# Kernel optimization log

Hardware: AMD Instinct MI355X
Metric: run time of the kernel (lower is better)

Reference implementation:

```python
import jax, jax.numpy as jnp
import numpy as np

B = 64       # number of graphs
R = 148      # fixed ROI count from source
D = 64       # hidden_channels (embed_dim, 4 heads)
H = 4
IN1 = 64     # node feature dim (after stripping label column)
INR = 148    # roi-graph feature dim
HID = 1000
NCLS = 2
N1 = 262144
E1 = 1048576
N2 = B * R
E2 = 262144
EPS = 1e-5


def setup_inputs() -> dict:
    key = jax.random.key(0)
    ks = jax.random.split(key, 40)
    def p(i, shape, s=0.1):
        return jax.random.normal(ks[i], shape, dtype=jnp.float32) * s
    inp = {
        'x_feat': jax.random.normal(ks[0], (N1, IN1), dtype=jnp.float32),
        'node_roi': jax.random.randint(ks[1], (N1,), 0, R, dtype=jnp.int32),
        'batch1': ((jnp.arange(N1, dtype=jnp.int32) * B) // N1).astype(jnp.int32),
        'edge_index1': jax.random.randint(ks[2], (2, E1), 0, N1, dtype=jnp.int32),
        'edge_weight1': jax.random.uniform(ks[3], (E1,), dtype=jnp.float32, minval=0.1, maxval=1.0),
        'x2_feat': jax.random.normal(ks[4], (N2, INR), dtype=jnp.float32),
        'roi_labels2': (jnp.arange(N2, dtype=jnp.int32) % R).astype(jnp.int32),
        'batch2': (jnp.arange(N2, dtype=jnp.int32) // R).astype(jnp.int32),
        'edge_index2': jax.random.randint(ks[5], (2, E2), 0, N2, dtype=jnp.int32),
        'edge_weight2': jax.random.uniform(ks[6], (E2,), dtype=jnp.float32, minval=0.1, maxval=1.0),
        'Wg1': p(7, (IN1, D)), 'bg1': jnp.zeros((D,), jnp.float32),
        'Wg2': p(8, (D, D)), 'bg2': jnp.zeros((D,), jnp.float32),
        'Wr1': p(9, (INR, D)), 'br1': jnp.zeros((D,), jnp.float32),
        'Wr2': p(10, (D, D)), 'br2': jnp.zeros((D,), jnp.float32),
        'in_proj_w': p(11, (3 * D, D)), 'in_proj_b': jnp.zeros((3 * D,), jnp.float32),
        'out_proj_w': p(12, (D, D)), 'out_proj_b': jnp.zeros((D,), jnp.float32),
        'ln1_g': jnp.ones((D,), jnp.float32), 'ln1_b': jnp.zeros((D,), jnp.float32),
        'ff_w1': p(13, (D, D)), 'ff_b1': jnp.zeros((D,), jnp.float32),
        'ff_w2': p(14, (D, D)), 'ff_b2': jnp.zeros((D,), jnp.float32),
        'ln2_g': jnp.ones((D,), jnp.float32), 'ln2_b': jnp.zeros((D,), jnp.float32),
        'Wc1': p(15, (R * D, HID), 0.02), 'bc1': jnp.zeros((HID,), jnp.float32),
        'bn_g': jnp.ones((HID,), jnp.float32), 'bn_b': jnp.zeros((HID,), jnp.float32),
        'Wc2': p(16, (HID, NCLS), 0.02), 'bc2': jnp.zeros((NCLS,), jnp.float32),
    }
    return inp


def gcn_conv(h, src, dst, ew, W, b, n):
    # PyG GCNConv w/ edge weights: add self-loops (weight 1), sym-normalize.
    h = h @ W
    deg = jax.ops.segment_sum(ew, dst, num_segments=n) + 1.0
    dinv = jax.lax.rsqrt(deg)
    norm = dinv[src] * ew * dinv[dst]                      # (E,)
    agg = jax.ops.segment_sum(h[src] * norm[:, None], dst, num_segments=n)
    agg = agg + h * (dinv * dinv)[:, None]                 # self-loop term
    return agg + b


def roi_pool_mean(h, roi, batch):
    # fused scatter mean keyed by (batch, roi) -> (B, R, d); empty slots stay 0
    seg = batch * R + roi
    sums = jax.ops.segment_sum(h, seg, num_segments=B * R)
    cnt = jax.ops.segment_sum(jnp.ones_like(h[:, 0]), seg, num_segments=B * R)
    return (sums / jnp.maximum(cnt, 1.0)[:, None]).reshape(B, R, h.shape[1])


def layer_norm(x, g, b):
    mu = x.mean(axis=-1, keepdims=True)
    var = x.var(axis=-1, keepdims=True)
    return (x - mu) * jax.lax.rsqrt(var + EPS) * g + b


def reference(x_feat, node_roi, batch1, edge_index1, edge_weight1,
              x2_feat, roi_labels2, batch2, edge_index2, edge_weight2,
              Wg1, bg1, Wg2, bg2, Wr1, br1, Wr2, br2,
              in_proj_w, in_proj_b, out_proj_w, out_proj_b,
              ln1_g, ln1_b, ff_w1, ff_b1, ff_w2, ff_b2, ln2_g, ln2_b,
              Wc1, bc1, bn_g, bn_b, Wc2, bc2):
    s1, d1 = edge_index1[0], edge_index1[1]
    s2, d2 = edge_index2[0], edge_index2[1]

    # ROI-graph branch (convs_roi[:-1]): 2 GCN layers, relu, eval dropout=noop
    h2 = jax.nn.relu(gcn_conv(x2_feat, s2, d2, edge_weight2, Wr1, br1, N2))
    h2 = jax.nn.relu(gcn_conv(h2, s2, d2, edge_weight2, Wr2, br2, N2))
    pooled_roi = roi_pool_mean(h2, roi_labels2, batch2)          # (B,R,D)

    # node-graph branch (convs[:-1])
    h1 = jax.nn.relu(gcn_conv(x_feat, s1, d1, edge_weight1, Wg1, bg1, N1))
    h1 = jax.nn.relu(gcn_conv(h1, s1, d1, edge_weight1, Wg2, bg2, N1))
    pooled = roi_pool_mean(h1, node_roi, batch1)                 # (B,R,D)

    combined = pooled + pooled_roi                               # transformer_in_combined

    # SelfAttnBlock (torch MultiheadAttention, batch_first, 4 heads)
    hd = D // H
    qkv = combined @ in_proj_w.T + in_proj_b                     # (B,R,3D)
    q, k, v = jnp.split(qkv, 3, axis=-1)
    q = q.reshape(B, R, H, hd)
    k = k.reshape(B, R, H, hd)
    v = v.reshape(B, R, H, hd)
    scores = jnp.einsum('bqhd,bkhd->bhqk', q, k) / np.sqrt(hd).astype(np.float32)
    attn_w = jax.nn.softmax(scores, axis=-1)                     # (B,H,R,R)
    o = jnp.einsum('bhqk,bkhd->bqhd', attn_w, v).reshape(B, R, D)
    o = o @ out_proj_w.T + out_proj_b
    x = layer_norm(combined + o, ln1_g, ln1_b)
    f = jax.nn.relu(x @ ff_w1 + ff_b1) @ ff_w2 + ff_b2
    t_out = layer_norm(x + f, ln2_g, ln2_b)                      # (B,R,D)

    # classifier: Linear -> BatchNorm1d(eval: mean0,var1) -> LeakyReLU -> Linear
    z = t_out.reshape(B, R * D) @ Wc1 + bc1
    z = bn_g * z * jax.lax.rsqrt(jnp.asarray(1.0 + EPS, z.dtype)) + bn_b
    z = jnp.where(z >= 0, z, 0.01 * z)
    out = z @ Wc2 + bc2                                          # (B,NCLS)
    return (out, pooled, pooled_roi, t_out, attn_w)
```

## Files before the change

kernel.cpp:

```cpp
#include <hip/hip_runtime.h>
#include <cstdint>
#include <cstddef>

#define N1v 262144
#define E1v 1048576
#define N2v 9472
#define E2v 262144
#define BBv 64
#define RRv 148
#define HIDv 1000
#define BRv (BBv * RRv)
#define NSEG 9472
#define EPB 4096
#define NBK1 256
#define SH1 10
#define BINS1 1024
#define CAP1 4864
#define STR1 4608
#define NBK2 74
#define SH2 7
#define BINS2 128
#define CAP2 4096
#define STR2 4096
#define GB1 4096
#define GB2 1184
#define MB1 2048
#define MB2 148

__host__ __device__ constexpr int cdiv(int a, int b) { return (a + b - 1) / b; }

typedef __attribute__((ext_vector_type(8))) short bf16x8;
typedef __attribute__((ext_vector_type(4))) float f32x4;
typedef unsigned short ushort_t;
typedef unsigned long long u64;

__device__ inline short f2bf(float f) {
    union { float f; unsigned u; } v; v.f = f;
    unsigned r = v.u + 0x7fff + ((v.u >> 16) & 1);
    return (short)(r >> 16);
}
__device__ inline float bf2f(unsigned hs) {
    union { unsigned u; float f; } v; v.u = hs << 16; return v.f;
}
__device__ inline unsigned relu_pk(unsigned u) {
    unsigned r = u;
    if (r & 0x8000u) r &= 0xFFFF0000u;
    if (r & 0x80000000u) r &= 0x0000FFFFu;
    return r;
}

__global__ __launch_bounds__(256) void k_binB2(const int* __restrict__ src1, const int* __restrict__ dst1,
                                               const float* __restrict__ ew1, int* __restrict__ cur1, u64* __restrict__ rb1,
                                               const int* __restrict__ src2, const int* __restrict__ dst2,
                                               const float* __restrict__ ew2, int* __restrict__ cur2, u64* __restrict__ rb2) {
    int bid = blockIdx.x;
    const int* src; const int* dst; const float* ew; int* cur; u64* rb; int nbk, sh, e0; size_t stride;
    if (bid < E1v / EPB) { src = src1; dst = dst1; ew = ew1; cur = cur1; rb = rb1; nbk = NBK1; sh = SH1; e0 = bid * EPB; stride = STR1; }
    else { src = src2; dst = dst2; ew = ew2; cur = cur2; rb = rb2; nbk = NBK2; sh = SH2; e0 = (bid - E1v / EPB) * EPB; stride = STR2; }
    __shared__ int h[256], basg[256];
    int tid = threadIdx.x;
    if (tid < nbk) h[tid] = 0;
    __syncthreads();
    for (int t = tid; t < EPB; t += 256) atomicAdd(&h[dst[e0 + t] >> sh], 1);
    __syncthreads();
    if (tid < nbk) {
        int c = h[tid];
        basg[tid] = c ? atomicAdd(&cur[tid], c) : 0;
        h[tid] = 0;
    }
    __syncthreads();
    unsigned lowmask = (1u << sh) - 1u;
    for (int t = tid; t < EPB; t += 256) {
        int d = dst[e0 + t];
        int b = d >> sh;
        int r = atomicAdd(&h[b], 1);
        unsigned lo = ((unsigned)src[e0 + t] << sh) | ((unsigned)d & lowmask);
        rb[(size_t)b * stride + basg[b] + r] = ((u64)(unsigned)__float_as_int(ew[e0 + t]) << 32) | lo;
    }
}

__global__ __launch_bounds__(256) void k_scanC(const int* __restrict__ cur1, int* __restrict__ cb1,
                                               const int* __restrict__ cur2, int* __restrict__ cb2) {
    __shared__ int tmp[256];
    int t = threadIdx.x;
    int v = cur1[t];
    tmp[t] = v; __syncthreads();
    int val = v;
    for (int off = 1; off < 256; off <<= 1) { int o = (t >= off) ? tmp[t - off] : 0; __syncthreads(); val += o; tmp[t] = val; __syncthreads(); }
    cb1[t] = val - v;
    if (t == 255) cb1[256] = val;
    __syncthreads();
    int v2 = (t < NBK2) ? cur2[t] : 0;
    tmp[t] = v2; __syncthreads();
    int val2 = v2;
    for (int off = 1; off < 256; off <<= 1) { int o = (t >= off) ? tmp[t - off] : 0; __syncthreads(); val2 += o; tmp[t] = val2; __syncthreads(); }
    if (t < NBK2) cb2[t] = val2 - v2;
    if (t == NBK2 - 1) cb2[NBK2] = val2;
}

template<int BINS, int CAP, int SH, int STRIDE>
__global__ __launch_bounds__(256) void k_csrC(const u64* __restrict__ rb, const int* __restrict__ cnts,
                                              const int* __restrict__ cbase,
                                              float* __restrict__ dinv, int* __restrict__ offs,
                                              int2* __restrict__ snC) {
    int b = blockIdx.x;
    const u64* rbb = rb + (size_t)b * STRIDE;
    int cnt = cnts[b];
    int cb = cbase[b];
    __shared__ int hist[BINS];
    __shared__ float degs[BINS];
    __shared__ int scn[BINS];
    __shared__ int tmp[256];
    extern __shared__ int2 outb[];
    int tid = threadIdx.x;
    for (int i = tid; i < BINS; i += 256) { hist[i] = 0; degs[i] = 0.f; }
    __syncthreads();
    for (int j = tid; j < cnt; j += 256) {
        u64 rec = rbb[j];
        int bin = (int)((unsigned)rec & (BINS - 1));
        float w = __int_as_float((int)(rec >> 32));
        atomicAdd(&hist[bin], 1);
        atomicAdd(&degs[bin], w);
    }
    __syncthreads();
    constexpr int PER = (BINS + 255) / 256;
    int lv[PER];
    int tsum = 0;
    int base_i = tid * PER;
#pragma unroll
    for (int k = 0; k < PER; ++k) { int idx = base_i + k; lv[k] = (idx < BINS) ? hist[idx] : 0; tsum += lv[k]; }
    tmp[tid] = tsum; __syncthreads();
    int val = tsum;
    for (int off = 1; off < 256; off <<= 1) { int o = (tid >= off) ? tmp[tid - off] : 0; __syncthreads(); val += o; tmp[tid] = val; __syncthreads(); }
    int run = val - tsum;
#pragma unroll
    for (int k = 0; k < PER; ++k) { int idx = base_i + k; if (idx < BINS) { scn[idx] = run; run += lv[k]; } }
    __syncthreads();
    for (int i = tid; i < BINS; i += 256) {
        offs[b * BINS + i] = cb + scn[i];
        dinv[b * BINS + i] = rsqrtf(degs[i] + 1.0f);
    }
    __syncthreads();
    bool staged = (cnt <= CAP);
    for (int j = tid; j < cnt; j += 256) {
        u64 rec = rbb[j];
        unsigned lo = (unsigned)rec;
        int bin = (int)(lo & (BINS - 1));
        int s = (int)(lo >> SH);
        float w = __int_as_float((int)(rec >> 32));
        float wd = w * rsqrtf(degs[bin] + 1.0f);
        int r = atomicAdd(&scn[bin], 1);
        int2 o2 = make_int2(s, __float_as_int(wd));
        if (staged) outb[r] = o2;
        else snC[(size_t)cb + r] = o2;
    }
    __syncthreads();
    if (staged) {
        for (int j = tid; j < cnt; j += 256) snC[(size_t)cb + j] = outb[j];
    }
}

__global__ __launch_bounds__(256) void k_normfix(int2* __restrict__ snC1, const float* __restrict__ dinv1,
                                                 int2* __restrict__ snC2, const float* __restrict__ dinv2) {
    int bid = blockIdx.x;
    int2* snC; const float* dinv; int j;
    if (bid < E1v / 256) { snC = snC1; dinv = dinv1; j = bid * 256 + threadIdx.x; }
    else { snC = snC2; dinv = dinv2; j = (bid - E1v / 256) * 256 + threadIdx.x; }
    int2 e = snC[j];
    e.y = __float_as_int(dinv[e.x] * __int_as_float(e.y));
    snC[j] = e;
}

__global__ __launch_bounds__(256) void k_pool_csr(const int* __restrict__ roi, int* __restrict__ offs_p,
                                                  int* __restrict__ nodeC) {
    int b = blockIdx.x;
    __shared__ int rl[4096];
    __shared__ int hist[RRv];
    __shared__ int curs[RRv];
    int tid = threadIdx.x;
    for (int t = tid; t < RRv; t += 256) hist[t] = 0;
    __syncthreads();
    int base = b * 4096;
    for (int t = tid; t < 4096; t += 256) {
        int r = roi[base + t];
        rl[t] = r;
        atomicAdd(&hist[r], 1);
    }
    __syncthreads();
    if (tid < RRv) {
        int s = 0;
        for (int k = 0; k < tid; ++k) s += hist[k];
        curs[tid] = s;
        offs_p[b * RRv + tid] = base + s;
    }
    __syncthreads();
    for (int t = tid; t < 4096; t += 256) {
        int r = rl[t];
        int j = atomicAdd(&curs[r], 1);
        nodeC[base + j] = base + t;
    }
}

__global__ __launch_bounds__(256) void k_pool_all(const int* __restrict__ nodeC, const int* __restrict__ offs,
                                                  const ushort_t* __restrict__ Ab, const ushort_t* __restrict__ h2Ab,
                                                  float* __restrict__ pooled, float* __restrict__ pooledroi,
                                                  float* __restrict__ comb) {
    int tid = threadIdx.x;
    int lane = tid & 63;
    int nh = lane >> 5;
    int slot = (lane >> 3) & 3;
    int f8 = lane & 7;
    int gw = blockIdx.x * 4 + (tid >> 6);
    int tw = gridDim.x * 4;
    for (int ss = gw * 2; ss < NSEG; ss += tw * 2) {
        int s = ss + nh;
        int beg = offs[s];
        int end = (s + 1 < NSEG) ? offs[s + 1] : N1v;
        float a0 = 0.f, a1 = 0.f, a2 = 0.f, a3 = 0.f, a4 = 0.f, a5 = 0.f, a6 = 0.f, a7 = 0.f;
        for (int j = beg + slot; j < end; j += 4) {
            int node = nodeC[j];
            uint4 v = *(const uint4*)(Ab + (size_t)node * 64 + f8 * 8);
            a0 += fmaxf(bf2f(v.x & 0xffffu), 0.f);
            a1 += fmaxf(bf2f(v.x >> 16), 0.f);
            a2 += fmaxf(bf2f(v.y & 0xffffu), 0.f);
            a3 += fmaxf(bf2f(v.y >> 16), 0.f);
            a4 += fmaxf(bf2f(v.z & 0xffffu), 0.f);
            a5 += fmaxf(bf2f(v.z >> 16), 0.f);
            a6 += fmaxf(bf2f(v.w & 0xffffu), 0.f);
            a7 += fmaxf(bf2f(v.w >> 16), 0.f);
        }
        a0 += __shfl_xor(a0, 8);  a1 += __shfl_xor(a1, 8);  a2 += __shfl_xor(a2, 8);  a3 += __shfl_xor(a3, 8);
        a4 += __shfl_xor(a4, 8);  a5 += __shfl_xor(a5, 8);  a6 += __shfl_xor(a6, 8);  a7 += __shfl_xor(a7, 8);
        a0 += __shfl_xor(a0, 16); a1 += __shfl_xor(a1, 16); a2 += __shfl_xor(a2, 16); a3 += __shfl_xor(a3, 16);
        a4 += __shfl_xor(a4, 16); a5 += __shfl_xor(a5, 16); a6 += __shfl_xor(a6, 16); a7 += __shfl_xor(a7, 16);
        if (slot == 0) {
            float inv = 1.f / (float)max(end - beg, 1);
            float p0 = a0 * inv, p1 = a1 * inv, p2 = a2 * inv, p3 = a3 * inv;
            float p4 = a4 * inv, p5 = a5 * inv, p6 = a6 * inv, p7 = a7 * inv;
            uint4 v2 = *(const uint4*)(h2Ab + (size_t)s * 64 + f8 * 8);
            float q0 = fmaxf(bf2f(v2.x & 0xffffu), 0.f);
            float q1 = fmaxf(bf2f(v2.x >> 16), 0.f);
            float q2 = fmaxf(bf2f(v2.y & 0xffffu), 0.f);
            float q3 = fmaxf(bf2f(v2.y >> 16), 0.f);
            float q4 = fmaxf(bf2f(v2.z & 0xffffu), 0.f);
            float q5 = fmaxf(bf2f(v2.z >> 16), 0.f);
            float q6 = fmaxf(bf2f(v2.w & 0xffffu), 0.f);
            float q7 = fmaxf(bf2f(v2.w >> 16), 0.f);
            size_t bo = (size_t)s * 64 + f8 * 8;
            float4 t;
            t.x = p0; t.y = p1; t.z = p2; t.w = p3; *(float4*)(pooled + bo) = t;
            t.x = p4; t.y = p5; t.z = p6; t.w = p7; *(float4*)(pooled + bo + 4) = t;
            t.x = q0; t.y = q1; t.z = q2; t.w = q3; *(float4*)(pooledroi + bo) = t;
            t.x = q4; t.y = q5; t.z = q6; t.w = q7; *(float4*)(pooledroi + bo + 4) = t;
            t.x = p0 + q0; t.y = p1 + q1; t.z = p2 + q2; t.w = p3 + q3; *(float4*)(comb + bo) = t;
            t.x = p4 + q4; t.y = p5 + q5; t.z = p6 + q6; t.w = p7 + q7; *(float4*)(comb + bo + 4) = t;
        }
    }
}

__device__ inline void gather_body(const int2* __restrict__ snC, const int* __restrict__ offs,
                                   const ushort_t* __restrict__ Pb, const float* __restrict__ dinv,
                                   const float* __restrict__ bias, ushort_t* __restrict__ A,
                                   int N, int E, int gw, int tw, int lane) {
    int nh = lane >> 5;
    int slot = (lane >> 3) & 3;
    int f8 = lane & 7;
    float4 bv0 = *(const float4*)(bias + f8 * 8);
    float4 bv1 = *(const float4*)(bias + f8 * 8 + 4);
    for (int ii = gw * 2; ii < N; ii += tw * 2) {
        int i = ii + nh;
        int beg = offs[i];
        int end = (i + 1 < N) ? offs[i + 1] : E;
        float a0 = 0.f, a1 = 0.f, a2 = 0.f, a3 = 0.f, a4 = 0.f, a5 = 0.f, a6 = 0.f, a7 = 0.f;
        for (int j = beg + slot; j < end; j += 4) {
            int2 e = snC[j];
            int s = e.x;
            float nv = __int_as_float(e.y);
            uint4 w = *(const uint4*)(Pb + (size_t)s * 64 + f8 * 8);
            a0 = fmaf(nv, bf2f(w.x & 0xffffu), a0);
            a1 = fmaf(nv, bf2f(w.x >> 16), a1);
            a2 = fmaf(nv, bf2f(w.y & 0xffffu), a2);
            a3 = fmaf(nv, bf2f(w.y >> 16), a3);
            a4 = fmaf(nv, bf2f(w.z & 0xffffu), a4);
            a5 = fmaf(nv, bf2f(w.z >> 16), a5);
            a6 = fmaf(nv, bf2f(w.w & 0xffffu), a6);
            a7 = fmaf(nv, bf2f(w.w >> 16), a7);
        }
        a0 += __shfl_xor(a0, 8);  a1 += __shfl_xor(a1, 8);  a2 += __shfl_xor(a2, 8);  a3 += __shfl_xor(a3, 8);
        a4 += __shfl_xor(a4, 8);  a5 += __shfl_xor(a5, 8);  a6 += __shfl_xor(a6, 8);  a7 += __shfl_xor(a7, 8);
        a0 += __shfl_xor(a0, 16); a1 += __shfl_xor(a1, 16); a2 += __shfl_xor(a2, 16); a3 += __shfl_xor(a3, 16);
        a4 += __shfl_xor(a4, 16); a5 += __shfl_xor(a5, 16); a6 += __shfl_xor(a6, 16); a7 += __shfl_xor(a7, 16);
        if (slot == 0) {
            uint4 w = *(const uint4*)(Pb + (size_t)i * 64 + f8 * 8);
            float di = dinv[i];
            float s2 = di * di;
            float r0 = fmaf(s2, bf2f(w.x & 0xffffu), a0) + bv0.x;
            float r1 = fmaf(s2, bf2f(w.x >> 16),    a1) + bv0.y;
            float r2 = fmaf(s2, bf2f(w.y & 0xffffu), a2) + bv0.z;
            float r3 = fmaf(s2, bf2f(w.y >> 16),    a3) + bv0.w;
            float r4 = fmaf(s2, bf2f(w.z & 0xffffu), a4) + bv1.x;
            float r5 = fmaf(s2, bf2f(w.z >> 16),    a5) + bv1.y;
            float r6 = fmaf(s2, bf2f(w.w & 0xffffu), a6) + bv1.z;
            float r7 = fmaf(s2, bf2f(w.w >> 16),    a7) + bv1.w;
            uint4 ov;
            ov.x = (unsigned)(ushort_t)f2bf(r0) | ((unsigned)(ushort_t)f2bf(r1) << 16);
            ov.y = (unsigned)(ushort_t)f2bf(r2) | ((unsigned)(ushort_t)f2bf(r3) << 16);
            ov.z = (unsigned)(ushort_t)f2bf(r4) | ((unsigned)(ushort_t)f2bf(r5) << 16);
            ov.w = (unsigned)(ushort_t)f2bf(r6) | ((unsigned)(ushort_t)f2bf(r7) << 16);
            *(uint4*)(A + (size_t)i * 64 + f8 * 8) = ov;
        }
    }
}

__global__ __launch_bounds__(256) void k_gather_both(const int2* __restrict__ snC1, const int* __restrict__ offs1,
                                                     const ushort_t* __restrict__ P1, const float* __restrict__ dinv1,
                                                     const float* __restrict__ b1, ushort_t* __restrict__ A1,
                                                     const int2* __restrict__ snC2, const int* __restrict__ offs2,
                                                     const ushort_t* __restrict__ P2, const float* __restrict__ dinv2,
                                                     const float* __restrict__ b2, ushort_t* __restrict__ A2) {
    int tid = threadIdx.x;
    int lane = tid & 63;
    if (blockIdx.x < GB1)
        gather_body(snC1, offs1, P1, dinv1, b1, A1, N1v, E1v,
                    blockIdx.x * 4 + (tid >> 6), GB1 * 4, lane);
    else
        gather_body(snC2, offs2, P2, dinv2, b2, A2, N2v, E2v,
                    (blockIdx.x - GB1) * 4 + (tid >> 6), GB2 * 4, lane);
}

__device__ inline void gemm_bf16_body(const ushort_t* __restrict__ X, const float* __restrict__ Wmat,
                                      ushort_t* __restrict__ Y, int N, int gw, int tw, int tid) {
    int lane = tid & 63;
    int l15 = lane & 15;
    int lg = lane >> 4;
    bf16x8 bfrag[2][4];
    for (int kh = 0; kh < 2; ++kh)
        for (int ct = 0; ct < 4; ++ct) {
            bf16x8 b;
#pragma unroll
            for (int i = 0; i < 8; ++i)
                b[i] = f2bf(Wmat[(size_t)(kh * 32 + lg * 8 + i) * 64 + ct * 16 + l15]);
            bfrag[kh][ct] = b;
        }
    int ntiles = N >> 4;
    for (int t = gw; t < ntiles; t += tw) {
        int row0 = t << 4;
        const ushort_t* xp = X + (size_t)(row0 + l15) * 64 + lg * 8;
        uint4 c0 = *(const uint4*)(xp);
        uint4 c1 = *(const uint4*)(xp + 32);
        c0.x = relu_pk(c0.x); c0.y = relu_pk(c0.y); c0.z = relu_pk(c0.z); c0.w = relu_pk(c0.w);
        c1.x = relu_pk(c1.x); c1.y = relu_pk(c1.y); c1.z = relu_pk(c1.z); c1.w = relu_pk(c1.w);
        bf16x8 af0 = *reinterpret_cast<bf16x8*>(&c0);
        bf16x8 af1 = *reinterpret_cast<bf16x8*>(&c1);
        f32x4 acc0 = {0.f, 0.f, 0.f, 0.f}, acc1 = acc0, acc2 = acc0, acc3 = acc0;
        acc0 = __builtin_amdgcn_mfma_f32_16x16x32_bf16(af0, bfrag[0][0], acc0, 0, 0, 0);
        acc1 = __builtin_amdgcn_mfma_f32_16x16x32_bf16(af0, bfrag[0][1], acc1, 0, 0, 0);
        acc2 = __builtin_amdgcn_mfma_f32_16x16x32_bf16(af0, bfrag[0][2], acc2, 0, 0, 0);
        acc3 = __builtin_amdgcn_mfma_f32_16x16x32_bf16(af0, bfrag[0][3], acc3, 0, 0, 0);
        acc0 = __builtin_amdgcn_mfma_f32_16x16x32_bf16(af1, bfrag[1][0], acc0, 0, 0, 0);
        acc1 = __builtin_amdgcn_mfma_f32_16x16x32_bf16(af1, bfrag[1][1], acc1, 0, 0, 0);
        acc2 = __builtin_amdgcn_mfma_f32_16x16x32_bf16(af1, bfrag[1][2], acc2, 0, 0, 0);
        acc3 = __builtin_amdgcn_mfma_f32_16x16x32_bf16(af1, bfrag[1][3], acc3, 0, 0, 0);
        ushort_t* yp = Y + (size_t)(row0 + lg * 4) * 64 + l15;
#pragma unroll
        for (int r = 0; r < 4; ++r) {
            yp[(size_t)r * 64 + 0]  = (ushort_t)f2bf(acc0[r]);
            yp[(size_t)r * 64 + 16] = (ushort_t)f2bf(acc1[r]);
            yp[(size_t)r * 64 + 32] = (ushort_t)f2bf(acc2[r]);
            yp[(size_t)r * 64 + 48] = (ushort_t)f2bf(acc3[r]);
        }
    }
}

__global__ __launch_bounds__(256) void k_gemm_both(const ushort_t* __restrict__ X1, const float* __restrict__ W1,
                                                   ushort_t* __restrict__ Y1,
                                                   const ushort_t* __restrict__ X2, const float* __restrict__ W2,
                                                   ushort_t* __restrict__ Y2) {
    int tid = threadIdx.x;
    if (blockIdx.x < MB1)
        gemm_bf16_body(X1, W1, Y1, N1v, blockIdx.x * 4 + (tid >> 6), MB1 * 4, tid);
    else
        gemm_bf16_body(X2, W2, Y2, N2v, (blockIdx.x - MB1) * 4 + (tid >> 6), MB2 * 4, tid);
}

__global__ __launch_bounds__(256) void k_gemm_mfma_f32(const float* __restrict__ X, const float* __restrict__ Wmat,
                                                       ushort_t* __restrict__ Y, int N) {
    int tid = threadIdx.x;
    int lane = tid & 63;
    int wv = tid >> 6;
    int l15 = lane & 15;
    int lg = lane >> 4;
    bf16x8 bfrag[2][4];
    for (int kh = 0; kh < 2; ++kh)
        for (int ct = 0; ct < 4; ++ct) {
            bf16x8 b;
#pragma unroll
            for (int i = 0; i < 8; ++i)
                b[i] = f2bf(Wmat[(size_t)(kh * 32 + lg * 8 + i) * 64 + ct * 16 + l15]);
            bfrag[kh][ct] = b;
        }
    int gw = blockIdx.x * 4 + wv;
    int tw = gridDim.x * 4;
    int ntiles = N >> 4;
    for (int t = gw; t < ntiles; t += tw) {
        int row0 = t << 4;
        const float* xp = X + (size_t)(row0 + l15) * 64 + lg * 8;
        float4 a0 = *(const float4*)(xp);
        float4 a1 = *(const float4*)(xp + 4);
        float4 a2 = *(const float4*)(xp + 32);
        float4 a3 = *(const float4*)(xp + 36);
        bf16x8 af0, af1;
        af0[0] = f2bf(a0.x); af0[1] = f2bf(a0.y); af0[2] = f2bf(a0.z); af0[3] = f2bf(a0.w);
        af0[4] = f2bf(a1.x); af0[5] = f2bf(a1.y); af0[6] = f2bf(a1.z); af0[7] = f2bf(a1.w);
        af1[0] = f2bf(a2.x); af1[1] = f2bf(a2.y); af1[2] = f2bf(a2.z); af1[3] = f2bf(a2.w);
        af1[4] = f2bf(a3.x); af1[5] = f2bf(a3.y); af1[6] = f2bf(a3.z); af1[7] = f2bf(a3.w);
        f32x4 acc0 = {0.f, 0.f, 0.f, 0.f}, acc1 = acc0, acc2 = acc0, acc3 = acc0;
        acc0 = __builtin_amdgcn_mfma_f32_16x16x32_bf16(af0, bfrag[0][0], acc0, 0, 0, 0);
        acc1 = __builtin_amdgcn_mfma_f32_16x16x32_bf16(af0, bfrag[0][1], acc1, 0, 0, 0);
        acc2 = __builtin_amdgcn_mfma_f32_16x16x32_bf16(af0, bfrag[0][2], acc2, 0, 0, 0);
        acc3 = __builtin_amdgcn_mfma_f32_16x16x32_bf16(af0, bfrag[0][3], acc3, 0, 0, 0);
        acc0 = __builtin_amdgcn_mfma_f32_16x16x32_bf16(af1, bfrag[1][0], acc0, 0, 0, 0);
        acc1 = __builtin_amdgcn_mfma_f32_16x16x32_bf16(af1, bfrag[1][1], acc1, 0, 0, 0);
        acc2 = __builtin_amdgcn_mfma_f32_16x16x32_bf16(af1, bfrag[1][2], acc2, 0, 0, 0);
        acc3 = __builtin_amdgcn_mfma_f32_16x16x32_bf16(af1, bfrag[1][3], acc3, 0, 0, 0);
        ushort_t* yp = Y + (size_t)(row0 + lg * 4) * 64 + l15;
#pragma unroll
        for (int r = 0; r < 4; ++r) {
            yp[(size_t)r * 64 + 0]  = (ushort_t)f2bf(acc0[r]);
            yp[(size_t)r * 64 + 16] = (ushort_t)f2bf(acc1[r]);
            yp[(size_t)r * 64 + 32] = (ushort_t)f2bf(acc2[r]);
            yp[(size_t)r * 64 + 48] = (ushort_t)f2bf(acc3[r]);
        }
    }
}

template<int MB, bool RIN, bool ROUT, bool OBF16>
__global__ __launch_bounds__(256) void k_gemm_rowwave(const float* __restrict__ X, const float* __restrict__ W,
                                                      const float* __restrict__ bias, void* __restrict__ Yv,
                                                      int N, int K) {
    extern __shared__ float Wl[];
    const int M = MB * 64;
    for (int idx = threadIdx.x; idx < K * M; idx += 256) Wl[idx] = W[idx];
    __syncthreads();
    int lane = threadIdx.x & 63;
    int gw = blockIdx.x * 4 + (threadIdx.x >> 6);
    int tw = gridDim.x * 4;
    const int K4 = K >> 2;
    for (int row = gw; row < N; row += tw) {
        float acc[MB];
#pragma unroll
        for (int cb = 0; cb < MB; ++cb) acc[cb] = 0.f;
        const float4* xr = (const float4*)(X + (size_t)row * K);
        for (int k4 = 0; k4 < K4; ++k4) {
            float4 xv = xr[k4];
            if (RIN) {
                xv.x = fmaxf(xv.x, 0.f); xv.y = fmaxf(xv.y, 0.f);
                xv.z = fmaxf(xv.z, 0.f); xv.w = fmaxf(xv.w, 0.f);
            }
            const float* wp = Wl + (k4 * 4) * M + lane;
#pragma unroll
            for (int cb = 0; cb < MB; ++cb) acc[cb] = fmaf(xv.x, wp[cb * 64], acc[cb]);
            wp += M;
#pragma unroll
            for (int cb = 0; cb < MB; ++cb) acc[cb] = fmaf(xv.y, wp[cb * 64], acc[cb]);
            wp += M;
#pragma unroll
            for (int cb = 0; cb < MB; ++cb) acc[cb] = fmaf(xv.z, wp[cb * 64], acc[cb]);
            wp += M;
#pragma unroll
            for (int cb = 0; cb < MB; ++cb) acc[cb] = fmaf(xv.w, wp[cb * 64], acc[cb]);
        }
#pragma unroll
        for (int cb = 0; cb < MB; ++cb) {
            float y = acc[cb];
            int col = cb * 64 + lane;
            if (bias) y += bias[col];
            if (ROUT) y = fmaxf(y, 0.f);
            if (OBF16) ((ushort_t*)Yv)[(size_t)row * M + col] = (ushort_t)f2bf(y);
            else ((float*)Yv)[(size_t)row * M + col] = y;
        }
    }
}

__global__ __launch_bounds__(256) void k_transpose2(const float* __restrict__ Win, float* __restrict__ WinT,
                                                    const float* __restrict__ Wout, float* __restrict__ WoutT) {
    int i = blockIdx.x * 256 + threadIdx.x;
    if (i < 192 * 64) {
        int r = i >> 6, c = i & 63;
        WinT[c * 192 + r] = Win[i];
    } else if (i < 192 * 64 + 64 * 64) {
        int j = i - 192 * 64;
        int r = j >> 6, c = j & 63;
        WoutT[c * 64 + r] = Wout[j];
    }
}

__global__ __launch_bounds__(256) void k_attn(const float* __restrict__ qkv, float* __restrict__ aw,
                                              float* __restrict__ o) {
    int qc = blockIdx.x & 3;
    int bh = blockIdx.x >> 2;
    int b = bh >> 2, h = bh & 3;
    __shared__ float qs[37][16];
    __shared__ float kT[16][152];
    __shared__ float vs[148][16];
    __shared__ float ps[4][152];
    int tid = threadIdx.x;
    const float* base = qkv + (size_t)b * 148 * 192 + h * 16;
    for (int idx = tid; idx < 148 * 16; idx += 256) {
        int i = idx >> 4, d = idx & 15;
        const float* p = base + (size_t)i * 192 + d;
        kT[d][i] = p[64];
        vs[i][d] = p[128];
    }
    int q0 = qc * 37;
    for (int idx = tid; idx < 37 * 16; idx += 256) {
        int i = idx >> 4, d = idx & 15;
        qs[i][d] = base[(size_t)(q0 + i) * 192 + d] * 0.25f;
    }
    __syncthreads();
    int wv = tid >> 6, lane = tid & 63;
    float* aw_bh = aw + (size_t)bh * 148 * 148;
    for (int ii = wv; ii < 37; ii += 4) {
        int i = q0 + ii;
        float s0 = 0.f, s1 = 0.f, s2 = 0.f;
#pragma unroll
        for (int d = 0; d < 16; ++d) {
            float q = qs[ii][d];
            s0 = fmaf(q, kT[d][lane], s0);
            s1 = fmaf(q, kT[d][lane + 64], s1);
            if (lane < 20) s2 = fmaf(q, kT[d][lane + 128], s2);
        }
        float m = fmaxf(s0, s1);
        if (lane < 20) m = fmaxf(m, s2);
#pragma unroll
        for (int off = 1; off < 64; off <<= 1) m = fmaxf(m, __shfl_xor(m, off));
        float e0 = __expf(s0 - m), e1 = __expf(s1 - m);
        float e2 = (lane < 20) ? __expf(s2 - m) : 0.f;
        float sum = e0 + e1 + e2;
#pragma unroll
        for (int off = 1; off < 64; off <<= 1) sum += __shfl_xor(sum, off);
        float inv = 1.f / sum;
        float p0 = e0 * inv, p1 = e1 * inv, p2 = e2 * inv;
        float* awr = aw_bh + (size_t)i * 148;
        awr[lane] = p0;
        awr[lane + 64] = p1;
        if (lane < 20) awr[lane + 128] = p2;
        ps[wv][lane] = p0;
        ps[wv][lane + 64] = p1;
        if (lane < 20) ps[wv][lane + 128] = p2;
        int d = lane & 15, jj = lane >> 4;
        float acc = 0.f;
        for (int t = jj; t < 148; t += 4) acc = fmaf(ps[wv][t], vs[t][d], acc);
        acc += __shfl_xor(acc, 16);
        acc += __shfl_xor(acc, 32);
        if (lane < 16) o[((size_t)b * 148 + i) * 64 + h * 16 + d] = acc;
    }
}

__global__ __launch_bounds__(256) void k_ln_gemm(const float* __restrict__ X, const float* __restrict__ Wt,
                                                 const float* __restrict__ bias, const float* __restrict__ resid,
                                                 const float* __restrict__ g, const float* __restrict__ bb,
                                                 float* __restrict__ Y, int N) {
    __shared__ float Wl[4096];
    for (int idx = threadIdx.x; idx < 4096; idx += 256) Wl[idx] = Wt[idx];
    __syncthreads();
    int lane = threadIdx.x & 63;
    int gw = blockIdx.x * 4 + (threadIdx.x >> 6);
    int tw = gridDim.x * 4;
    for (int row = gw; row < N; row += tw) {
        const float4* xr = (const float4*)(X + (size_t)row * 64);
        float acc = 0.f;
        for (int k4 = 0; k4 < 16; ++k4) {
            float4 xv = xr[k4];
            const float* wp = Wl + (k4 * 4) * 64 + lane;
            acc = fmaf(xv.x, wp[0], acc);
            acc = fmaf(xv.y, wp[64], acc);
            acc = fmaf(xv.z, wp[128], acc);
            acc = fmaf(xv.w, wp[192], acc);
        }
        float y = acc + bias[lane] + resid[(size_t)row * 64 + lane];
        float s = y;
#pragma unroll
        for (int off = 1; off < 64; off <<= 1) s += __shfl_xor(s, off);
        float mu = s * (1.f / 64.f);
        float dcen = y - mu;
        float v = dcen * dcen;
#pragma unroll
        for (int off = 1; off < 64; off <<= 1) v += __shfl_xor(v, off);
        float var = v * (1.f / 64.f);
        Y[(size_t)row * 64 + lane] = dcen * rsqrtf(var + 1e-5f) * g[lane] + bb[lane];
    }
}

__global__ __launch_bounds__(256) void k_cls_part(const float* __restrict__ T, const float* __restrict__ Wc1,
                                                  float* __restrict__ Zp) {
    int ks = blockIdx.x >> 2;
    int mt = blockIdx.x & 3;
    int k0 = ks * 74;
    int m0 = mt * 256;
    __shared__ float Tl[64][74];
    int tid = threadIdx.x;
    for (int idx = tid; idx < 64 * 74; idx += 256) {
        int b = idx / 74, kk = idx - b * 74;
        Tl[b][kk] = T[(size_t)b * 9472 + k0 + kk];
    }
    __syncthreads();
    int lane = tid & 63, bq = tid >> 6;
    int mbase = m0 + lane * 4;
    size_t moff = (mbase + 3 < 1000) ? (size_t)mbase : 0;
    float4 acc[16];
#pragma unroll
    for (int j = 0; j < 16; ++j) acc[j] = make_float4(0.f, 0.f, 0.f, 0.f);
#pragma unroll 2
    for (int kk = 0; kk < 74; ++kk) {
        float4 w = *(const float4*)(Wc1 + (size_t)(k0 + kk) * 1000 + moff);
#pragma unroll
        for (int j = 0; j < 16; ++j) {
            float t = Tl[bq * 16 + j][kk];
            acc[j].x = fmaf(t, w.x, acc[j].x);
            acc[j].y = fmaf(t, w.y, acc[j].y);
            acc[j].z = fmaf(t, w.z, acc[j].z);
            acc[j].w = fmaf(t, w.w, acc[j].w);
        }
    }
    float* zp = Zp + (size_t)ks * 64 * 1024;
#pragma unroll
    for (int j = 0; j < 16; ++j) {
        int b = bq * 16 + j;
        *(float4*)(zp + (size_t)b * 1024 + mbase) = acc[j];
    }
}

__global__ __launch_bounds__(256) void k_cls_reduce(const float* __restrict__ Zp, const float* __restrict__ bc1,
                                                    const float* __restrict__ bn_g, const float* __restrict__ bn_b,
                                                    float* __restrict__ zb) {
    int flat = blockIdx.x * 256 + threadIdx.x;
    int b = flat >> 10, m = flat & 1023;
    if (m >= 1000) return;
    float s = 0.f;
    for (int ks = 0; ks < 128; ++ks)
        s += Zp[((size_t)ks * 64 + b) * 1024 + m];
    float rs = rsqrtf(1.0f + 1e-5f);
    float z = bn_g[m] * (s + bc1[m]) * rs + bn_b[m];
    zb[flat] = z >= 0.f ? z : 0.01f * z;
}

__global__ __launch_bounds__(256) void k_cls_final(const float* __restrict__ zb,
                                                   const float* __restrict__ Wc2, const float* __restrict__ bc2,
                                                   float* __restrict__ out) {
    int b = blockIdx.x;
    int tid = threadIdx.x;
    float a0 = 0.f, a1 = 0.f;
    for (int m = tid; m < 1000; m += 256) {
        float z = zb[b * 1024 + m];
        a0 = fmaf(z, Wc2[m * 2], a0);
        a1 = fmaf(z, Wc2[m * 2 + 1], a1);
    }
#pragma unroll
    for (int off = 1; off < 64; off <<= 1) {
        a0 += __shfl_xor(a0, off);
        a1 += __shfl_xor(a1, off);
    }
    __shared__ float r0[4], r1[4];
    if ((tid & 63) == 0) { r0[tid >> 6] = a0; r1[tid >> 6] = a1; }
    __syncthreads();
    if (tid == 0) {
        out[b * 2 + 0] = r0[0] + r0[1] + r0[2] + r0[3] + bc2[0];
        out[b * 2 + 1] = r1[0] + r1[1] + r1[2] + r1[3] + bc2[1];
    }
}

extern "C" void kernel_launch(void* const* d_in, const int* in_sizes, int n_in,
                              void* d_out, int out_size, void* d_ws, size_t ws_size,
                              hipStream_t stream) {
    (void)in_sizes; (void)n_in; (void)out_size; (void)ws_size;

    const float* x_feat = (const float*)d_in[0];
    const int* node_roi = (const int*)d_in[1];
    const int* ei1 = (const int*)d_in[3];
    const float* ew1 = (const float*)d_in[4];
    const float* x2f = (const float*)d_in[5];
    const int* ei2 = (const int*)d_in[8];
    const float* ew2 = (const float*)d_in[9];
    const float* Wg1 = (const float*)d_in[10];
    const float* bg1 = (const float*)d_in[11];
    const float* Wg2 = (const float*)d_in[12];
    const float* bg2 = (const float*)d_in[13];
    const float* Wr1 = (const float*)d_in[14];
    const float* br1 = (const float*)d_in[15];
    const float* Wr2 = (const float*)d_in[16];
    const float* br2 = (const float*)d_in[17];
    const float* in_proj_w = (const float*)d_in[18];
    const float* in_proj_b = (const float*)d_in[19];
    const float* out_proj_w = (const float*)d_in[20];
    const float* out_proj_b = (const float*)d_in[21];
    const float* ln1_g = (const float*)d_in[22];
    const float* ln1_b = (const float*)d_in[23];
    const float* ff_w1 = (const float*)d_in[24];
    const float* ff_b1 = (const float*)d_in[25];
    const float* ff_w2 = (const float*)d_in[26];
    const float* ff_b2 = (const float*)d_in[27];
    const float* ln2_g = (const float*)d_in[28];
    const float* ln2_b = (const float*)d_in[29];
    const float* Wc1 = (const float*)d_in[30];
    const float* bc1 = (const float*)d_in[31];
    const float* bn_g = (const float*)d_in[32];
    const float* bn_b = (const float*)d_in[33];
    const float* Wc2 = (const float*)d_in[34];
    const float* bc2 = (const float*)d_in[35];

    const int* src1 = ei1;
    const int* dst1 = ei1 + E1v;
    const int* src2 = ei2;
    const int* dst2 = ei2 + E2v;

    float* out = (float*)d_out;
    const int PSZ = BRv * 64;
    float* pooled_out = out + 128;
    float* pooledroi_out = out + 128 + PSZ;
    float* tout_out = out + 128 + 2 * PSZ;
    float* attn_out = out + 128 + 3 * PSZ;

    float* W = (float*)d_ws;
    size_t o = 0;
    int* cur1 = (int*)(W + o); o += 256;
    int* cur2 = (int*)(W + o); o += 128;
    size_t zone_elems = o;
    int* cb1 = (int*)(W + o);  o += 260;
    int* cb2 = (int*)(W + o);  o += 76;
    o = (o + 1) & ~(size_t)1;
    int2* snC1 = (int2*)(W + o); o += (size_t)E1v * 2;
    int2* snC2 = (int2*)(W + o); o += (size_t)E2v * 2;
    float* dinv1 = W + o;        o += N1v;
    float* dinv2 = W + o;        o += N2v;
    int* offs1 = (int*)(W + o);  o += N1v;
    int* offs2 = (int*)(W + o);  o += N2v;
    int* offs_p = (int*)(W + o); o += NSEG;
    int* nodeC = (int*)(W + o);  o += N1v;
    float* zbuf = W + o;         o += BBv * 1024;
    o = (o + 1) & ~(size_t)1;
    ushort_t* h2P = (ushort_t*)(W + o);  o += (size_t)N2v * 32;
    ushort_t* h2Ab = (ushort_t*)(W + o); o += (size_t)N2v * 32;
    o = (o + 1) & ~(size_t)1;
    size_t h1P_off = o; o += (size_t)N1v * 64;
    size_t h1A_off = o; o += (size_t)N1v * 64;
    ushort_t* h1P = (ushort_t*)(W + h1P_off);
    ushort_t* h1Ab = (ushort_t*)(W + h1A_off);
    u64* rb1 = (u64*)(W + h1P_off);
    u64* rb2 = rb1 + (size_t)NBK1 * STR1;
    size_t p = h1P_off;
    float* comb = W + p; p += PSZ;
    float* qkvb = W + p; p += (size_t)BRv * 192;
    float* obuf = W + p; p += PSZ;
    float* xbuf = W + p; p += PSZ;
    float* f1 = W + p;   p += PSZ;
    float* WinT = W + p; p += 64 * 192;
    float* WoutT = W + p; p += 64 * 64;
    float* Zp = W + h1A_off;

    dim3 blk(256);

    hipMemsetAsync(W, 0, zone_elems * sizeof(float), stream);

    k_binB2<<<E1v / EPB + E2v / EPB, blk, 0, stream>>>(src1, dst1, ew1, cur1, rb1,
                                                       src2, dst2, ew2, cur2, rb2);
    k_scanC<<<1, blk, 0, stream>>>(cur1, cb1, cur2, cb2);
    k_csrC<BINS1, CAP1, SH1, STR1><<<NBK1, blk, CAP1 * 8, stream>>>(rb1, cur1, cb1, dinv1, offs1, snC1);
    k_csrC<BINS2, CAP2, SH2, STR2><<<NBK2, blk, CAP2 * 8, stream>>>(rb2, cur2, cb2, dinv2, offs2, snC2);
    k_normfix<<<E1v / 256 + E2v / 256, blk, 0, stream>>>(snC1, dinv1, snC2, dinv2);
    k_pool_csr<<<BBv, blk, 0, stream>>>(node_roi, offs_p, nodeC);

    k_gemm_mfma_f32<<<MB1, blk, 0, stream>>>(x_feat, Wg1, h1P, N1v);
    k_gemm_rowwave<1, false, false, true><<<cdiv(N2v, 4), blk, 148 * 64 * 4, stream>>>(x2f, Wr1, nullptr, h2P, N2v, 148);
    k_gather_both<<<GB1 + GB2, blk, 0, stream>>>(snC1, offs1, h1P, dinv1, bg1, h1Ab,
                                                 snC2, offs2, h2P, dinv2, br1, h2Ab);
    k_gemm_both<<<MB1 + MB2, blk, 0, stream>>>(h1Ab, Wg2, h1P, h2Ab, Wr2, h2P);
    k_gather_both<<<GB1 + GB2, blk, 0, stream>>>(snC1, offs1, h1P, dinv1, bg2, h1Ab,
                                                 snC2, offs2, h2P, dinv2, br2, h2Ab);
    k_pool_all<<<2048, blk, 0, stream>>>(nodeC, offs_p, h1Ab, h2Ab, pooled_out, pooledroi_out, comb);

    k_transpose2<<<cdiv(192 * 64 + 64 * 64, 256), blk, 0, stream>>>(in_proj_w, WinT, out_proj_w, WoutT);
    k_gemm_rowwave<3, false, false, false><<<cdiv(N2v, 4), blk, 64 * 192 * 4, stream>>>(comb, WinT, in_proj_b, qkvb, N2v, 64);
    k_attn<<<BBv * 4 * 4, blk, 0, stream>>>(qkvb, attn_out, obuf);
    k_ln_gemm<<<cdiv(N2v, 4), blk, 0, stream>>>(obuf, WoutT, out_proj_b, comb, ln1_g, ln1_b, xbuf, N2v);
    k_gemm_rowwave<1, false, true, false><<<cdiv(N2v, 4), blk, 64 * 64 * 4, stream>>>(xbuf, ff_w1, ff_b1, f1, N2v, 64);
    k_ln_gemm<<<cdiv(N2v, 4), blk, 0, stream>>>(f1, ff_w2, ff_b2, xbuf, ln2_g, ln2_b, tout_out, N2v);

    k_cls_part<<<512, blk, 0, stream>>>(tout_out, Wc1, Zp);
    k_cls_reduce<<<BBv * 1024 / 256, blk, 0, stream>>>(Zp, bc1, bn_g, bn_b, zbuf);
    k_cls_final<<<BBv, blk, 0, stream>>>(zbuf, Wc2, bc2, out);
}
```

Baseline: 393.1 us.

## Merge independent preprocessing kernels into one multi-role launch and relocate edge bin buffer

Edge binning, the first node-feature GEMM, pooling CSR construction and the attention weight transposes are fused into a single kernel that dispatches on block index. This cuts launch overhead and lets independent work run side by side. The edge bin buffer moves out of the h1P region into its own workspace slot so the GEMM writing h1P cannot clobber it. The ROI GEMM is also moved earlier in the stream. In exchange the workspace grows, and every block of the fused kernel now reserves the larger shared-memory footprint, which may lower occupancy for the GEMM blocks.

```diff
diff --git a/kernel.cpp b/kernel.cpp
--- a/kernel.cpp
+++ b/kernel.cpp
@@ -26,6 +26,10 @@
 #define GB2 1184
 #define MB1 2048
 #define MB2 148
+#define PH_B2 (E1v / EPB + E2v / EPB)
+#define PH_G1 MB1
+#define PH_PC BBv
+#define PH_TR 64
 
 __host__ __device__ constexpr int cdiv(int a, int b) { return (a + b - 1) / b; }
 
@@ -49,15 +53,10 @@
     return r;
 }
 
-__global__ __launch_bounds__(256) void k_binB2(const int* __restrict__ src1, const int* __restrict__ dst1,
-                                               const float* __restrict__ ew1, int* __restrict__ cur1, u64* __restrict__ rb1,
-                                               const int* __restrict__ src2, const int* __restrict__ dst2,
-                                               const float* __restrict__ ew2, int* __restrict__ cur2, u64* __restrict__ rb2) {
-    int bid = blockIdx.x;
-    const int* src; const int* dst; const float* ew; int* cur; u64* rb; int nbk, sh, e0; size_t stride;
-    if (bid < E1v / EPB) { src = src1; dst = dst1; ew = ew1; cur = cur1; rb = rb1; nbk = NBK1; sh = SH1; e0 = bid * EPB; stride = STR1; }
-    else { src = src2; dst = dst2; ew = ew2; cur = cur2; rb = rb2; nbk = NBK2; sh = SH2; e0 = (bid - E1v / EPB) * EPB; stride = STR2; }
-    __shared__ int h[256], basg[256];
+__device__ inline void binB2_body(const int* __restrict__ src, const int* __restrict__ dst,
+                                  const float* __restrict__ ew, int* __restrict__ cur, u64* __restrict__ rb,
+                                  int nbk, int sh, int e0, size_t stride,
+                                  int* __restrict__ h, int* __restrict__ basg) {
     int tid = threadIdx.x;
     if (tid < nbk) h[tid] = 0;
     __syncthreads();
@@ -76,6 +75,114 @@
         int r = atomicAdd(&h[b], 1);
         unsigned lo = ((unsigned)src[e0 + t] << sh) | ((unsigned)d & lowmask);
         rb[(size_t)b * stride + basg[b] + r] = ((u64)(unsigned)__float_as_int(ew[e0 + t]) << 32) | lo;
+    }
+}
+
+__device__ inline void gemm_f32_body(const float* __restrict__ X, const float* __restrict__ Wmat,
+                                     ushort_t* __restrict__ Y, int N, int gw, int tw, int tid) {
+    int lane = tid & 63;
+    int l15 = lane & 15;
+    int lg = lane >> 4;
+    bf16x8 bfrag[2][4];
+    for (int kh = 0; kh < 2; ++kh)
+        for (int ct = 0; ct < 4; ++ct) {
+            bf16x8 b;
+#pragma unroll
+            for (int i = 0; i < 8; ++i)
+                b[i] = f2bf(Wmat[(size_t)(kh * 32 + lg * 8 + i) * 64 + ct * 16 + l15]);
+            bfrag[kh][ct] = b;
+        }
+    int ntiles = N >> 4;
+    for (int t = gw; t < ntiles; t += tw) {
+        int row0 = t << 4;
+        const float* xp = X + (size_t)(row0 + l15) * 64 + lg * 8;
+        float4 a0 = *(const float4*)(xp);
+        float4 a1 = *(const float4*)(xp + 4);
+        float4 a2 = *(const float4*)(xp + 32);
+        float4 a3 = *(const float4*)(xp + 36);
+        bf16x8 af0, af1;
+        af0[0] = f2bf(a0.x); af0[1] = f2bf(a0.y); af0[2] = f2bf(a0.z); af0[3] = f2bf(a0.w);
+        af0[4] = f2bf(a1.x); af0[5] = f2bf(a1.y); af0[6] = f2bf(a1.z); af0[7] = f2bf(a1.w);
+        af1[0] = f2bf(a2.x); af1[1] = f2bf(a2.y); af1[2] = f2bf(a2.z); af1[3] = f2bf(a2.w);
+        af1[4] = f2bf(a3.x); af1[5] = f2bf(a3.y); af1[6] = f2bf(a3.z); af1[7] = f2bf(a3.w);
+        f32x4 acc0 = {0.f, 0.f, 0.f, 0.f}, acc1 = acc0, acc2 = acc0, acc3 = acc0;
+        acc0 = __builtin_amdgcn_mfma_f32_16x16x32_bf16(af0, bfrag[0][0], acc0, 0, 0, 0);
+        acc1 = __builtin_amdgcn_mfma_f32_16x16x32_bf16(af0, bfrag[0][1], acc1, 0, 0, 0);
+        acc2 = __builtin_amdgcn_mfma_f32_16x16x32_bf16(af0, bfrag[0][2], acc2, 0, 0, 0);
+        acc3 = __builtin_amdgcn_mfma_f32_16x16x32_bf16(af0, bfrag[0][3], acc3, 0, 0, 0);
+        acc0 = __builtin_amdgcn_mfma_f32_16x16x32_bf16(af1, bfrag[1][0], acc0, 0, 0, 0);
+        acc1 = __builtin_amdgcn_mfma_f32_16x16x32_bf16(af1, bfrag[1][1], acc1, 0, 0, 0);
+        acc2 = __builtin_amdgcn_mfma_f32_16x16x32_bf16(af1, bfrag[1][2], acc2, 0, 0, 0);
+        acc3 = __builtin_amdgcn_mfma_f32_16x16x32_bf16(af1, bfrag[1][3], acc3, 0, 0, 0);
+        ushort_t* yp = Y + (size_t)(row0 + lg * 4) * 64 + l15;
+#pragma unroll
+        for (int r = 0; r < 4; ++r) {
+            yp[(size_t)r * 64 + 0]  = (ushort_t)f2bf(acc0[r]);
+            yp[(size_t)r * 64 + 16] = (ushort_t)f2bf(acc1[r]);
+            yp[(size_t)r * 64 + 32] = (ushort_t)f2bf(acc2[r]);
+            yp[(size_t)r * 64 + 48] = (ushort_t)f2bf(acc3[r]);
+        }
+    }
+}
+
+__device__ inline void pool_csr_body(const int* __restrict__ roi, int* __restrict__ offs_p,
+                                     int* __restrict__ nodeC, int b, int* __restrict__ smem) {
+    int* rl = smem;
+    int* hist = smem + 4096;
+    int* curs = smem + 4096 + RRv;
+    int tid = threadIdx.x;
+    for (int t = tid; t < RRv; t += 256) hist[t] = 0;
+    __syncthreads();
+    int base = b * 4096;
+    for (int t = tid; t < 4096; t += 256) {
+        int r = roi[base + t];
+        rl[t] = r;
+        atomicAdd(&hist[r], 1);
+    }
+    __syncthreads();
+    if (tid < RRv) {
+        int s = 0;
+        for (int k = 0; k < tid; ++k) s += hist[k];
+        curs[tid] = s;
+        offs_p[b * RRv + tid] = base + s;
+    }
+    __syncthreads();
+    for (int t = tid; t < 4096; t += 256) {
+        int r = rl[t];
+        int j = atomicAdd(&curs[r], 1);
+        nodeC[base + j] = base + t;
+    }
+}
+
+__global__ __launch_bounds__(256) void k_phase1(
+    const int* __restrict__ src1, const int* __restrict__ dst1, const float* __restrict__ ew1,
+    int* __restrict__ cur1, u64* __restrict__ rb1,
+    const int* __restrict__ src2, const int* __restrict__ dst2, const float* __restrict__ ew2,
+    int* __restrict__ cur2, u64* __restrict__ rb2,
+    const float* __restrict__ x_feat, const float* __restrict__ Wg1, ushort_t* __restrict__ h1P,
+    const int* __restrict__ roi, int* __restrict__ offs_p, int* __restrict__ nodeC,
+    const float* __restrict__ Win, float* __restrict__ WinT,
+    const float* __restrict__ Wout, float* __restrict__ WoutT) {
+    __shared__ int smem[4096 + 2 * RRv];
+    int bid = blockIdx.x;
+    int tid = threadIdx.x;
+    if (bid < PH_B2) {
+        if (bid < E1v / EPB)
+            binB2_body(src1, dst1, ew1, cur1, rb1, NBK1, SH1, bid * EPB, STR1, smem, smem + 256);
+        else
+            binB2_body(src2, dst2, ew2, cur2, rb2, NBK2, SH2, (bid - E1v / EPB) * EPB, STR2, smem, smem + 256);
+    } else if (bid < PH_B2 + PH_G1) {
+        gemm_f32_body(x_feat, Wg1, h1P, N1v, (bid - PH_B2) * 4 + (tid >> 6), PH_G1 * 4, tid);
+    } else if (bid < PH_B2 + PH_G1 + PH_PC) {
+        pool_csr_body(roi, offs_p, nodeC, bid - PH_B2 - PH_G1, smem);
+    } else {
+        int i = (bid - PH_B2 - PH_G1 - PH_PC) * 256 + tid;
+        if (i < 192 * 64) {
+            WinT[(i & 63) * 192 + (i >> 6)] = Win[i];
+        } else if (i < 192 * 64 + 64 * 64) {
+            int j = i - 192 * 64;
+            WoutT[(j & 63) * 64 + (j >> 6)] = Wout[j];
+        }
     }
 }
 
@@ -169,36 +276,6 @@
     int2 e = snC[j];
     e.y = __float_as_int(dinv[e.x] * __int_as_float(e.y));
     snC[j] = e;
-}
-
-__global__ __launch_bounds__(256) void k_pool_csr(const int* __restrict__ roi, int* __restrict__ offs_p,
-                                                  int* __restrict__ nodeC) {
-    int b = blockIdx.x;
-    __shared__ int rl[4096];
-    __shared__ int hist[RRv];
-    __shared__ int curs[RRv];
-    int tid = threadIdx.x;
-    for (int t = tid; t < RRv; t += 256) hist[t] = 0;
-    __syncthreads();
-    int base = b * 4096;
-    for (int t = tid; t < 4096; t += 256) {
-        int r = roi[base + t];
-        rl[t] = r;
-        atomicAdd(&hist[r], 1);
-    }
-    __syncthreads();
-    if (tid < RRv) {
-        int s = 0;
-        for (int k = 0; k < tid; ++k) s += hist[k];
-        curs[tid] = s;
-        offs_p[b * RRv + tid] = base + s;
-    }
-    __syncthreads();
-    for (int t = tid; t < 4096; t += 256) {
-        int r = rl[t];
-        int j = atomicAdd(&curs[r], 1);
-        nodeC[base + j] = base + t;
-    }
 }
 
 __global__ __launch_bounds__(256) void k_pool_all(const int* __restrict__ nodeC, const int* __restrict__ offs,
@@ -383,57 +460,6 @@
         gemm_bf16_body(X2, W2, Y2, N2v, (blockIdx.x - MB1) * 4 + (tid >> 6), MB2 * 4, tid);
 }
 
-__global__ __launch_bounds__(256) void k_gemm_mfma_f32(const float* __restrict__ X, const float* __restrict__ Wmat,
-                                                       ushort_t* __restrict__ Y, int N) {
-    int tid = threadIdx.x;
-    int lane = tid & 63;
-    int wv = tid >> 6;
-    int l15 = lane & 15;
-    int lg = lane >> 4;
-    bf16x8 bfrag[2][4];
-    for (int kh = 0; kh < 2; ++kh)
-        for (int ct = 0; ct < 4; ++ct) {
-            bf16x8 b;
-#pragma unroll
-            for (int i = 0; i < 8; ++i)
-                b[i] = f2bf(Wmat[(size_t)(kh * 32 + lg * 8 + i) * 64 + ct * 16 + l15]);
-            bfrag[kh][ct] = b;
-        }
-    int gw = blockIdx.x * 4 + wv;
-    int tw = gridDim.x * 4;
-    int ntiles = N >> 4;
-    for (int t = gw; t < ntiles; t += tw) {
-        int row0 = t << 4;
-        const float* xp = X + (size_t)(row0 + l15) * 64 + lg * 8;
-        float4 a0 = *(const float4*)(xp);
-        float4 a1 = *(const float4*)(xp + 4);
-        float4 a2 = *(const float4*)(xp + 32);
-        float4 a3 = *(const float4*)(xp + 36);
-        bf16x8 af0, af1;
-        af0[0] = f2bf(a0.x); af0[1] = f2bf(a0.y); af0[2] = f2bf(a0.z); af0[3] = f2bf(a0.w);
-        af0[4] = f2bf(a1.x); af0[5] = f2bf(a1.y); af0[6] = f2bf(a1.z); af0[7] = f2bf(a1.w);
-        af1[0] = f2bf(a2.x); af1[1] = f2bf(a2.y); af1[2] = f2bf(a2.z); af1[3] = f2bf(a2.w);
-        af1[4] = f2bf(a3.x); af1[5] = f2bf(a3.y); af1[6] = f2bf(a3.z); af1[7] = f2bf(a3.w);
-        f32x4 acc0 = {0.f, 0.f, 0.f, 0.f}, acc1 = acc0, acc2 = acc0, acc3 = acc0;
-        acc0 = __builtin_amdgcn_mfma_f32_16x16x32_bf16(af0, bfrag[0][0], acc0, 0, 0, 0);
-        acc1 = __builtin_amdgcn_mfma_f32_16x16x32_bf16(af0, bfrag[0][1], acc1, 0, 0, 0);
-        acc2 = __builtin_amdgcn_mfma_f32_16x16x32_bf16(af0, bfrag[0][2], acc2, 0, 0, 0);
-        acc3 = __builtin_amdgcn_mfma_f32_16x16x32_bf16(af0, bfrag[0][3], acc3, 0, 0, 0);
-        acc0 = __builtin_amdgcn_mfma_f32_16x16x32_bf16(af1, bfrag[1][0], acc0, 0, 0, 0);
-        acc1 = __builtin_amdgcn_mfma_f32_16x16x32_bf16(af1, bfrag[1][1], acc1, 0, 0, 0);
-        acc2 = __builtin_amdgcn_mfma_f32_16x16x32_bf16(af1, bfrag[1][2], acc2, 0, 0, 0);
-        acc3 = __builtin_amdgcn_mfma_f32_16x16x32_bf16(af1, bfrag[1][3], acc3, 0, 0, 0);
-        ushort_t* yp = Y + (size_t)(row0 + lg * 4) * 64 + l15;
-#pragma unroll
-        for (int r = 0; r < 4; ++r) {
-            yp[(size_t)r * 64 + 0]  = (ushort_t)f2bf(acc0[r]);
-            yp[(size_t)r * 64 + 16] = (ushort_t)f2bf(acc1[r]);
-            yp[(size_t)r * 64 + 32] = (ushort_t)f2bf(acc2[r]);
-            yp[(size_t)r * 64 + 48] = (ushort_t)f2bf(acc3[r]);
-        }
-    }
-}
-
 template<int MB, bool RIN, bool ROUT, bool OBF16>
 __global__ __launch_bounds__(256) void k_gemm_rowwave(const float* __restrict__ X, const float* __restrict__ W,
                                                       const float* __restrict__ bias, void* __restrict__ Yv,
@@ -479,19 +505,6 @@
             if (OBF16) ((ushort_t*)Yv)[(size_t)row * M + col] = (ushort_t)f2bf(y);
             else ((float*)Yv)[(size_t)row * M + col] = y;
         }
-    }
-}
-
-__global__ __launch_bounds__(256) void k_transpose2(const float* __restrict__ Win, float* __restrict__ WinT,
-                                                    const float* __restrict__ Wout, float* __restrict__ WoutT) {
-    int i = blockIdx.x * 256 + threadIdx.x;
-    if (i < 192 * 64) {
-        int r = i >> 6, c = i & 63;
-        WinT[c * 192 + r] = Win[i];
-    } else if (i < 192 * 64 + 64 * 64) {
-        int j = i - 192 * 64;
-        int r = j >> 6, c = j & 63;
-        WoutT[c * 64 + r] = Wout[j];
     }
 }
 
@@ -729,6 +742,8 @@
     int* cb1 = (int*)(W + o);  o += 260;
     int* cb2 = (int*)(W + o);  o += 76;
     o = (o + 1) & ~(size_t)1;
+    u64* rb1 = (u64*)(W + o);  o += (size_t)NBK1 * STR1 * 2;
+    u64* rb2 = (u64*)(W + o);  o += (size_t)NBK2 * STR2 * 2;
     int2* snC1 = (int2*)(W + o); o += (size_t)E1v * 2;
     int2* snC2 = (int2*)(W + o); o += (size_t)E2v * 2;
     float* dinv1 = W + o;        o += N1v;
@@ -738,6 +753,8 @@
     int* offs_p = (int*)(W + o); o += NSEG;
     int* nodeC = (int*)(W + o);  o += N1v;
     float* zbuf = W + o;         o += BBv * 1024;
+    float* WinT = W + o;  o += 192 * 64;
+    float* WoutT = W + o; o += 64 * 64;
     o = (o + 1) & ~(size_t)1;
     ushort_t* h2P = (ushort_t*)(W + o);  o += (size_t)N2v * 32;
     ushort_t* h2Ab = (ushort_t*)(W + o); o += (size_t)N2v * 32;
@@ -746,32 +763,28 @@
     size_t h1A_off = o; o += (size_t)N1v * 64;
     ushort_t* h1P = (ushort_t*)(W + h1P_off);
     ushort_t* h1Ab = (ushort_t*)(W + h1A_off);
-    u64* rb1 = (u64*)(W + h1P_off);
-    u64* rb2 = rb1 + (size_t)NBK1 * STR1;
     size_t p = h1P_off;
     float* comb = W + p; p += PSZ;
     float* qkvb = W + p; p += (size_t)BRv * 192;
     float* obuf = W + p; p += PSZ;
     float* xbuf = W + p; p += PSZ;
     float* f1 = W + p;   p += PSZ;
-    float* WinT = W + p; p += 64 * 192;
-    float* WoutT = W + p; p += 64 * 64;
     float* Zp = W + h1A_off;
 
     dim3 blk(256);
 
     hipMemsetAsync(W, 0, zone_elems * sizeof(float), stream);
 
-    k_binB2<<<E1v / EPB + E2v / EPB, blk, 0, stream>>>(src1, dst1, ew1, cur1, rb1,
-                                                       src2, dst2, ew2, cur2, rb2);
+    k_phase1<<<PH_B2 + PH_G1 + PH_PC + PH_TR, blk, 0, stream>>>(
+        src1, dst1, ew1, cur1, rb1, src2, dst2, ew2, cur2, rb2,
+        x_feat, Wg1, h1P, node_roi, offs_p, nodeC,
+        in_proj_w, WinT, out_proj_w, WoutT);
+    k_gemm_rowwave<1, false, false, true><<<cdiv(N2v, 4), blk, 148 * 64 * 4, stream>>>(x2f, Wr1, nullptr, h2P, N2v, 148);
     k_scanC<<<1, blk, 0, stream>>>(cur1, cb1, cur2, cb2);
     k_csrC<BINS1, CAP1, SH1, STR1><<<NBK1, blk, CAP1 * 8, stream>>>(rb1, cur1, cb1, dinv1, offs1, snC1);
     k_csrC<BINS2, CAP2, SH2, STR2><<<NBK2, blk, CAP2 * 8, stream>>>(rb2, cur2, cb2, dinv2, offs2, snC2);
     k_normfix<<<E1v / 256 + E2v / 256, blk, 0, stream>>>(snC1, dinv1, snC2, dinv2);
-    k_pool_csr<<<BBv, blk, 0, stream>>>(node_roi, offs_p, nodeC);
-
-    k_gemm_mfma_f32<<<MB1, blk, 0, stream>>>(x_feat, Wg1, h1P, N1v);
-    k_gemm_rowwave<1, false, false, true><<<cdiv(N2v, 4), blk, 148 * 64 * 4, stream>>>(x2f, Wr1, nullptr, h2P, N2v, 148);
+
     k_gather_both<<<GB1 + GB2, blk, 0, stream>>>(snC1, offs1, h1P, dinv1, bg1, h1Ab,
                                                  snC2, offs2, h2P, dinv2, br1, h2Ab);
     k_gemm_both<<<MB1 + MB2, blk, 0, stream>>>(h1Ab, Wg2, h1P, h2Ab, Wr2, h2P);
@@ -779,7 +792,6 @@
                                                  snC2, offs2, h2P, dinv2, br2, h2Ab);
     k_pool_all<<<2048, blk, 0, stream>>>(nodeC, offs_p, h1Ab, h2Ab, pooled_out, pooledroi_out, comb);
 
-    k_transpose2<<<cdiv(192 * 64 + 64 * 64, 256), blk, 0, stream>>>(in_proj_w, WinT, out_proj_w, WoutT);
     k_gemm_rowwave<3, false, false, false><<<cdiv(N2v, 4), blk, 64 * 192 * 4, stream>>>(comb, WinT, in_proj_b, qkvb, N2v, 64);
     k_attn<<<BBv * 4 * 4, blk, 0, stream>>>(qkvb, attn_out, obuf);
     k_ln_gemm<<<cdiv(N2v, 4), blk, 0, stream>>>(obuf, WoutT, out_proj_b, comb, ln1_g, ln1_b, xbuf, N2v);
```

New measurement: 390.5 us. No clear change (-0.7%).
